# Kernel tuning notes

Hardware: AMD Instinct MI355X
Metric: run time of the kernel (lower is better)

Reference implementation:

```python
import jax, jax.numpy as jnp
import numpy as np

TOP_K = 2
NUM_EXPERTS = 64
AUX_COEF = 0.01


def setup_inputs() -> dict:
    key = jax.random.key(0)
    kx, kw = jax.random.split(key)
    B, S, D, E = 4, 4096, 2048, NUM_EXPERTS
    x = jax.random.normal(kx, (B, S, D), dtype=jnp.float32)
    # nn.Linear default init ~ U(-1/sqrt(D), 1/sqrt(D))
    W = jax.random.uniform(kw, (E, D), dtype=jnp.float32,
                           minval=-1.0 / np.sqrt(D), maxval=1.0 / np.sqrt(D))
    return {"x": x, "W": W}


def reference(x, W):
    B, S, D = x.shape
    E = W.shape[0]
    # router projection (no bias)
    logits = jnp.einsum('bsd,ed->bse', x, W)          # [B,S,E]
    probs = jax.nn.softmax(logits, axis=-1)           # [B,S,E]
    top_k_gates, top_k_indices = jax.lax.top_k(probs, TOP_K)  # [B,S,K]
    top_k_gates = top_k_gates / (jnp.sum(top_k_gates, axis=-1, keepdims=True) + 1e-9)
    # aux loss: fraction of routed slots per expert (one-hot mean) x mean router prob
    total_slots = B * S * TOP_K
    counts = jnp.zeros((E,), dtype=jnp.float32).at[top_k_indices.reshape(-1)].add(1.0)
    avg_tokens_per_expert = counts / total_slots      # == one_hot(idx).mean(dims 0,1,2)
    avg_router_prob = jnp.mean(probs, axis=(0, 1))    # [E]
    aux_loss = AUX_COEF * E * jnp.sum(avg_tokens_per_expert * avg_router_prob)
    return top_k_indices, top_k_gates, aux_loss
```

## Files before the change

### kernel.cpp

```cpp
#include <hip/hip_runtime.h>
#include <math.h>

#define NTOK 16384
#define DDIM 2048
#define NEXP 64
#define TM   16
#define NBLK (NTOK / TM)
#define NCH  32
#define NS   64

typedef _Float16 half4v __attribute__((ext_vector_type(4)));
typedef _Float16 half8v __attribute__((ext_vector_type(8)));
typedef float    f32x4  __attribute__((ext_vector_type(4)));

#define MFMA16(a, b, c) __builtin_amdgcn_mfma_f32_16x16x32_f16((a), (b), (c), 0, 0, 0)

__global__ __launch_bounds__(256) void prep_kernel(const float* __restrict__ W,
                                                   _Float16* __restrict__ Wh,
                                                   _Float16* __restrict__ Wl,
                                                   float* __restrict__ accg) {
    int idx = blockIdx.x * 256 + threadIdx.x;
    int e  = idx >> 8;
    int k0 = (idx & 255) << 3;
    const float* wp = W + (size_t)e * DDIM + k0;
    float4 w0 = *(const float4*)wp;
    float4 w1 = *(const float4*)(wp + 4);
    half8v h, l;
    h[0] = (_Float16)w0.x; l[0] = (_Float16)(w0.x - (float)h[0]);
    h[1] = (_Float16)w0.y; l[1] = (_Float16)(w0.y - (float)h[1]);
    h[2] = (_Float16)w0.z; l[2] = (_Float16)(w0.z - (float)h[2]);
    h[3] = (_Float16)w0.w; l[3] = (_Float16)(w0.w - (float)h[3]);
    h[4] = (_Float16)w1.x; l[4] = (_Float16)(w1.x - (float)h[4]);
    h[5] = (_Float16)w1.y; l[5] = (_Float16)(w1.y - (float)h[5]);
    h[6] = (_Float16)w1.z; l[6] = (_Float16)(w1.z - (float)h[6]);
    h[7] = (_Float16)w1.w; l[7] = (_Float16)(w1.w - (float)h[7]);
    int S = k0 >> 5, nb = e >> 4, nl = e & 15, q = (k0 >> 3) & 3;
    size_t off = (size_t)S * 2048 + nb * 512 + q * 128 + nl * 8;
    *(half8v*)&Wh[off] = h;
    *(half8v*)&Wl[off] = l;
    if (idx < 128) accg[idx] = 0.0f;
}

__device__ inline void cvt_store(_Float16* __restrict__ Hp, _Float16* __restrict__ Lp,
                                 int off, float4 v) {
    half4v h, l;
    h.x = (_Float16)v.x; l.x = (_Float16)(v.x - (float)h.x);
    h.y = (_Float16)v.y; l.y = (_Float16)(v.y - (float)h.y);
    h.z = (_Float16)v.z; l.z = (_Float16)(v.z - (float)h.z);
    h.w = (_Float16)v.w; l.w = (_Float16)(v.w - (float)h.w);
    *(half4v*)&Hp[off] = h;
    *(half4v*)&Lp[off] = l;
}

__global__ __launch_bounds__(256, 4) void router_kernel(
    const float* __restrict__ x, const _Float16* __restrict__ Wh,
    const _Float16* __restrict__ Wl, float* __restrict__ accg,
    float* __restrict__ out)
{
    __shared__ __align__(16) _Float16 Ah[2][1024];
    __shared__ __align__(16) _Float16 Al[2][1024];
    __shared__ float lgt[TM][NEXP + 1];
    __shared__ float cnt[NEXP];

    const int tid  = threadIdx.x;
    const int lane = tid & 63;
    const int wv   = __builtin_amdgcn_readfirstlane(tid >> 6);
    const int m0   = blockIdx.x * TM;

    if (tid < NEXP) cnt[tid] = 0.0f;

    const int tok0 = tid >> 4;
    const int kk0  = (tid & 15) * 4;
    const int s0   = kk0 >> 5, q0 = (kk0 >> 3) & 3, j00 = kk0 & 7;
    const int offA = (s0 * 64 + q0 * 16 + tok0) * 8 + j00;

    const float* gx = x + (size_t)(m0 + tok0) * DDIM + kk0;

    const _Float16* whp = Wh + wv * 512 + lane * 8;
    const _Float16* wlp = Wl + wv * 512 + lane * 8;

    f32x4 acc = {0.f, 0.f, 0.f, 0.f};

    float4 stg[4];
    #pragma unroll
    for (int i = 0; i < 4; ++i) stg[i] = *(const float4*)(gx + i * 64);
    half8v wbh[2], wbl[2];
    #pragma unroll
    for (int s = 0; s < 2; ++s) {
        wbh[s] = *(const half8v*)(whp + (size_t)s * 2048);
        wbl[s] = *(const half8v*)(wlp + (size_t)s * 2048);
    }

    for (int ch = 0; ch < NCH; ++ch) {
        const int p = ch & 1;
        const int b = ch & 3;
        cvt_store(&Ah[p][0], &Al[p][0], offA, stg[b]);
        const int cf = (ch + 4 < NCH) ? ch + 4 : 0;
        stg[b] = *(const float4*)(gx + cf * 64);
        asm volatile("s_waitcnt lgkmcnt(0)" ::: "memory");
        __builtin_amdgcn_s_barrier();
        #pragma unroll
        for (int s = 0; s < 2; ++s) {
            const int Sg  = ch * 2 + s;
            const int SgN = (Sg + 2) & (NS - 1);
            half8v ah = *(const half8v*)&Ah[p][(s * 64 + lane) * 8];
            half8v al = *(const half8v*)&Al[p][(s * 64 + lane) * 8];
            half8v bh = wbh[s], bl = wbl[s];
            wbh[s] = *(const half8v*)(whp + (size_t)SgN * 2048);
            wbl[s] = *(const half8v*)(wlp + (size_t)SgN * 2048);
            acc = MFMA16(al, bh, acc);
            acc = MFMA16(ah, bl, acc);
            acc = MFMA16(ah, bh, acc);
        }
    }

    {
        const int q  = lane >> 4;
        const int nl = lane & 15;
        #pragma unroll
        for (int r = 0; r < 4; ++r)
            lgt[q * 4 + r][wv * 16 + nl] = acc[r];
    }
    __syncthreads();

    if (tid < 128) {
        const int m = tid >> 3;
        const int j = tid & 7;
        float l[8];
        #pragma unroll
        for (int i = 0; i < 8; ++i) l[i] = lgt[m][j * 8 + i];

        float mx = l[0];
        #pragma unroll
        for (int i = 1; i < 8; ++i) mx = fmaxf(mx, l[i]);
        #pragma unroll
        for (int off = 1; off < 8; off <<= 1) mx = fmaxf(mx, __shfl_xor(mx, off, 8));

        float ev[8];
        float zs = 0.f;
        float v1 = -INFINITY, v2 = -INFINITY;
        int i1 = 0, i2 = 0;
        #pragma unroll
        for (int i = 0; i < 8; ++i) {
            ev[i] = __expf(l[i] - mx);
            zs += ev[i];
            int e = j * 8 + i;
            if (l[i] > v1)      { v2 = v1; i2 = i1; v1 = l[i]; i1 = e; }
            else if (l[i] > v2) { v2 = l[i]; i2 = e; }
        }
        #pragma unroll
        for (int off = 1; off < 8; off <<= 1) zs += __shfl_xor(zs, off, 8);

        #pragma unroll
        for (int off = 1; off < 8; off <<= 1) {
            float ov1 = __shfl_xor(v1, off, 8);
            int   oi1 = __shfl_xor(i1, off, 8);
            float ov2 = __shfl_xor(v2, off, 8);
            int   oi2 = __shfl_xor(i2, off, 8);
            bool afirst = (v1 > ov1) || (v1 == ov1 && i1 < oi1);
            if (afirst) {
                bool t = (v2 > ov1) || (v2 == ov1 && i2 < oi1);
                v2 = t ? v2 : ov1;
                i2 = t ? i2 : oi1;
            } else {
                bool t = (ov2 > v1) || (ov2 == v1 && oi2 < i1);
                v2 = t ? ov2 : v1;
                i2 = t ? oi2 : i1;
                v1 = ov1;
                i1 = oi1;
            }
        }

        const float invz = 1.0f / zs;
        if (j == 0) {
            float p1 = invz;
            float p2 = __expf(v2 - mx) * invz;
            float sden = p1 + p2 + 1e-9f;
            int tok = m0 + m;
            out[tok * 2 + 0] = (float)i1;
            out[tok * 2 + 1] = (float)i2;
            out[32768 + tok * 2 + 0] = p1 / sden;
            out[32768 + tok * 2 + 1] = p2 / sden;
            atomicAdd(&cnt[i1], 1.0f);
            atomicAdd(&cnt[i2], 1.0f);
        }

        #pragma unroll
        for (int i = 0; i < 8; ++i) lgt[m][j * 8 + i] = ev[i] * invz;
    }
    __syncthreads();

    if (tid < NEXP) {
        atomicAdd(&accg[tid], cnt[tid]);
    } else if (tid < 128) {
        int e = tid - 64;
        float s = 0.f;
        #pragma unroll
        for (int t = 0; t < TM; ++t) s += lgt[t][e];
        atomicAdd(&accg[64 + e], s);
    }
}

__global__ void finalize_kernel(const float* __restrict__ accg,
                                float* __restrict__ out)
{
    int t = threadIdx.x;
    float c = accg[t];
    float p = accg[64 + t];
    float term = (c / (float)(NTOK * 2)) * (p / (float)NTOK);
    #pragma unroll
    for (int off = 1; off < 64; off <<= 1) term += __shfl_xor(term, off, 64);
    if (t == 0) out[65536] = 0.01f * (float)NEXP * term;
}

extern "C" void kernel_launch(void* const* d_in, const int* in_sizes, int n_in,
                              void* d_out, int out_size, void* d_ws, size_t ws_size,
                              hipStream_t stream) {
    const float* x = (const float*)d_in[0];
    const float* W = (const float*)d_in[1];
    float* out  = (float*)d_out;
    float* accg = (float*)d_ws;
    _Float16* Wh = (_Float16*)(accg + 128);
    _Float16* Wl = Wh + (size_t)DDIM * NEXP;

    prep_kernel<<<64, 256, 0, stream>>>(W, Wh, Wl, accg);
    router_kernel<<<NBLK, 256, 0, stream>>>(x, Wh, Wl, accg, out);
    finalize_kernel<<<1, 64, 0, stream>>>(accg, out);
}
```

Baseline: 220.0 us.

## Load x directly into MFMA registers and split K across waves with LDS reduction

Each block now handles 32 tokens. Its four waves split into two token halves and two K halves, and each wave computes all 64 experts with four accumulators. The kernel drops the LDS staging of x and the per-chunk barriers: each lane loads its fp32 x fragment straight from global memory and converts it to hi/lo halves in registers. A final LDS pass adds the two K-half partial sums. The change removes barrier and LDS traffic and reuses each x fragment across four expert tiles, at the cost of more registers, lower occupancy (launch bounds drop to 2) and uncoalesced strided row loads of x.

```diff
diff --git a/kernel.cpp b/kernel.cpp
--- a/kernel.cpp
+++ b/kernel.cpp
@@ -4,12 +4,10 @@
 #define NTOK 16384
 #define DDIM 2048
 #define NEXP 64
-#define TM   16
-#define NBLK (NTOK / TM)
-#define NCH  32
-#define NS   64
-
-typedef _Float16 half4v __attribute__((ext_vector_type(4)));
+#define TMB  32
+#define NBLK (NTOK / TMB)
+#define NSW  32
+
 typedef _Float16 half8v __attribute__((ext_vector_type(8)));
 typedef float    f32x4  __attribute__((ext_vector_type(4)));
 
@@ -41,89 +39,117 @@
     if (idx < 128) accg[idx] = 0.0f;
 }
 
-__device__ inline void cvt_store(_Float16* __restrict__ Hp, _Float16* __restrict__ Lp,
-                                 int off, float4 v) {
-    half4v h, l;
-    h.x = (_Float16)v.x; l.x = (_Float16)(v.x - (float)h.x);
-    h.y = (_Float16)v.y; l.y = (_Float16)(v.y - (float)h.y);
-    h.z = (_Float16)v.z; l.z = (_Float16)(v.z - (float)h.z);
-    h.w = (_Float16)v.w; l.w = (_Float16)(v.w - (float)h.w);
-    *(half4v*)&Hp[off] = h;
-    *(half4v*)&Lp[off] = l;
-}
-
-__global__ __launch_bounds__(256, 4) void router_kernel(
+__global__ __launch_bounds__(256, 2) void router_kernel(
     const float* __restrict__ x, const _Float16* __restrict__ Wh,
     const _Float16* __restrict__ Wl, float* __restrict__ accg,
     float* __restrict__ out)
 {
-    __shared__ __align__(16) _Float16 Ah[2][1024];
-    __shared__ __align__(16) _Float16 Al[2][1024];
-    __shared__ float lgt[TM][NEXP + 1];
+    __shared__ float pacc[2][64][16];
+    __shared__ float lgt[TMB][NEXP + 1];
     __shared__ float cnt[NEXP];
 
     const int tid  = threadIdx.x;
     const int lane = tid & 63;
     const int wv   = __builtin_amdgcn_readfirstlane(tid >> 6);
-    const int m0   = blockIdx.x * TM;
+    const int th   = wv & 1;
+    const int qk   = wv >> 1;
+    const int m0   = blockIdx.x * TMB;
 
     if (tid < NEXP) cnt[tid] = 0.0f;
 
-    const int tok0 = tid >> 4;
-    const int kk0  = (tid & 15) * 4;
-    const int s0   = kk0 >> 5, q0 = (kk0 >> 3) & 3, j00 = kk0 & 7;
-    const int offA = (s0 * 64 + q0 * 16 + tok0) * 8 + j00;
-
-    const float* gx = x + (size_t)(m0 + tok0) * DDIM + kk0;
-
-    const _Float16* whp = Wh + wv * 512 + lane * 8;
-    const _Float16* wlp = Wl + wv * 512 + lane * 8;
-
-    f32x4 acc = {0.f, 0.f, 0.f, 0.f};
-
-    float4 stg[4];
-    #pragma unroll
-    for (int i = 0; i < 4; ++i) stg[i] = *(const float4*)(gx + i * 64);
-    half8v wbh[2], wbl[2];
-    #pragma unroll
-    for (int s = 0; s < 2; ++s) {
-        wbh[s] = *(const half8v*)(whp + (size_t)s * 2048);
-        wbl[s] = *(const half8v*)(wlp + (size_t)s * 2048);
-    }
-
-    for (int ch = 0; ch < NCH; ++ch) {
-        const int p = ch & 1;
-        const int b = ch & 3;
-        cvt_store(&Ah[p][0], &Al[p][0], offA, stg[b]);
-        const int cf = (ch + 4 < NCH) ? ch + 4 : 0;
-        stg[b] = *(const float4*)(gx + cf * 64);
-        asm volatile("s_waitcnt lgkmcnt(0)" ::: "memory");
-        __builtin_amdgcn_s_barrier();
-        #pragma unroll
-        for (int s = 0; s < 2; ++s) {
-            const int Sg  = ch * 2 + s;
-            const int SgN = (Sg + 2) & (NS - 1);
-            half8v ah = *(const half8v*)&Ah[p][(s * 64 + lane) * 8];
-            half8v al = *(const half8v*)&Al[p][(s * 64 + lane) * 8];
-            half8v bh = wbh[s], bl = wbl[s];
-            wbh[s] = *(const half8v*)(whp + (size_t)SgN * 2048);
-            wbl[s] = *(const half8v*)(wlp + (size_t)SgN * 2048);
-            acc = MFMA16(al, bh, acc);
-            acc = MFMA16(ah, bl, acc);
-            acc = MFMA16(ah, bh, acc);
-        }
-    }
+    const int row = m0 + th * 16 + (lane & 15);
+    const float* gxp = x + (size_t)row * DDIM + qk * 1024 + (lane >> 4) * 8;
+
+    const _Float16* wbh = Wh + (size_t)qk * (NSW * 2048) + lane * 8;
+    const _Float16* wbl = Wl + (size_t)qk * (NSW * 2048) + lane * 8;
+
+    f32x4 acc0 = {0.f,0.f,0.f,0.f}, acc1 = {0.f,0.f,0.f,0.f};
+    f32x4 acc2 = {0.f,0.f,0.f,0.f}, acc3 = {0.f,0.f,0.f,0.f};
+
+    float4 xA0 = *(const float4*)(gxp +   0), xB0 = *(const float4*)(gxp +   4);
+    float4 xA1 = *(const float4*)(gxp +  32), xB1 = *(const float4*)(gxp +  36);
+    float4 xA2 = *(const float4*)(gxp +  64), xB2 = *(const float4*)(gxp +  68);
+    float4 xA3 = *(const float4*)(gxp +  96), xB3 = *(const float4*)(gxp + 100);
+    half8v h0a = *(const half8v*)(wbh +    0), h1a = *(const half8v*)(wbh +  512);
+    half8v h2a = *(const half8v*)(wbh + 1024), h3a = *(const half8v*)(wbh + 1536);
+    half8v l0a = *(const half8v*)(wbl +    0), l1a = *(const half8v*)(wbl +  512);
+    half8v l2a = *(const half8v*)(wbl + 1024), l3a = *(const half8v*)(wbl + 1536);
+    half8v h0b = *(const half8v*)(wbh + 2048), h1b = *(const half8v*)(wbh + 2560);
+    half8v h2b = *(const half8v*)(wbh + 3072), h3b = *(const half8v*)(wbh + 3584);
+    half8v l0b = *(const half8v*)(wbl + 2048), l1b = *(const half8v*)(wbl + 2560);
+    half8v l2b = *(const half8v*)(wbl + 3072), l3b = *(const half8v*)(wbl + 3584);
+
+#define STEP(S, XA, XB, H0,H1,H2,H3, L0,L1,L2,L3)                           \
+    {                                                                        \
+        half8v ah, al;                                                       \
+        ah[0]=(_Float16)XA.x; al[0]=(_Float16)(XA.x-(float)ah[0]);           \
+        ah[1]=(_Float16)XA.y; al[1]=(_Float16)(XA.y-(float)ah[1]);           \
+        ah[2]=(_Float16)XA.z; al[2]=(_Float16)(XA.z-(float)ah[2]);           \
+        ah[3]=(_Float16)XA.w; al[3]=(_Float16)(XA.w-(float)ah[3]);           \
+        ah[4]=(_Float16)XB.x; al[4]=(_Float16)(XB.x-(float)ah[4]);           \
+        ah[5]=(_Float16)XB.y; al[5]=(_Float16)(XB.y-(float)ah[5]);           \
+        ah[6]=(_Float16)XB.z; al[6]=(_Float16)(XB.z-(float)ah[6]);           \
+        ah[7]=(_Float16)XB.w; al[7]=(_Float16)(XB.w-(float)ah[7]);           \
+        half8v bh0=H0, bl0=L0, bh1=H1, bl1=L1;                               \
+        half8v bh2=H2, bl2=L2, bh3=H3, bl3=L3;                               \
+        const int Sw_ = ((S) + 2 < NSW) ? (S) + 2 : 0;                       \
+        const _Float16* whs = wbh + (size_t)Sw_ * 2048;                      \
+        const _Float16* wls = wbl + (size_t)Sw_ * 2048;                      \
+        H0 = *(const half8v*)(whs +    0); L0 = *(const half8v*)(wls +    0);\
+        H1 = *(const half8v*)(whs +  512); L1 = *(const half8v*)(wls +  512);\
+        H2 = *(const half8v*)(whs + 1024); L2 = *(const half8v*)(wls + 1024);\
+        H3 = *(const half8v*)(whs + 1536); L3 = *(const half8v*)(wls + 1536);\
+        acc0 = MFMA16(al, bh0, acc0);                                        \
+        acc0 = MFMA16(ah, bl0, acc0);                                        \
+        acc0 = MFMA16(ah, bh0, acc0);                                        \
+        acc1 = MFMA16(al, bh1, acc1);                                        \
+        acc1 = MFMA16(ah, bl1, acc1);                                        \
+        acc1 = MFMA16(ah, bh1, acc1);                                        \
+        acc2 = MFMA16(al, bh2, acc2);                                        \
+        acc2 = MFMA16(ah, bl2, acc2);                                        \
+        acc2 = MFMA16(ah, bh2, acc2);                                        \
+        acc3 = MFMA16(al, bh3, acc3);                                        \
+        acc3 = MFMA16(ah, bl3, acc3);                                        \
+        acc3 = MFMA16(ah, bh3, acc3);                                        \
+        const int Sx_ = ((S) + 4 < NSW) ? (S) + 4 : 0;                       \
+        XA = *(const float4*)(gxp + Sx_ * 32);                               \
+        XB = *(const float4*)(gxp + Sx_ * 32 + 4);                           \
+    }
+
+    for (int s = 0; s < NSW; s += 4) {
+        STEP(s + 0, xA0, xB0, h0a,h1a,h2a,h3a, l0a,l1a,l2a,l3a);
+        STEP(s + 1, xA1, xB1, h0b,h1b,h2b,h3b, l0b,l1b,l2b,l3b);
+        STEP(s + 2, xA2, xB2, h0a,h1a,h2a,h3a, l0a,l1a,l2a,l3a);
+        STEP(s + 3, xA3, xB3, h0b,h1b,h2b,h3b, l0b,l1b,l2b,l3b);
+    }
+#undef STEP
+
+    if (wv >= 2) {
+        #pragma unroll
+        for (int r = 0; r < 4; ++r) {
+            pacc[th][lane][ 0 + r] = acc0[r];
+            pacc[th][lane][ 4 + r] = acc1[r];
+            pacc[th][lane][ 8 + r] = acc2[r];
+            pacc[th][lane][12 + r] = acc3[r];
+        }
+    }
+    __syncthreads();
+
+    if (wv < 2) {
+        const int qr = lane >> 4;
+        const int nl = lane & 15;
+        #pragma unroll
+        for (int r = 0; r < 4; ++r) {
+            const int m = th * 16 + qr * 4 + r;
+            lgt[m][ 0 + nl] = acc0[r] + pacc[th][lane][ 0 + r];
+            lgt[m][16 + nl] = acc1[r] + pacc[th][lane][ 4 + r];
+            lgt[m][32 + nl] = acc2[r] + pacc[th][lane][ 8 + r];
+            lgt[m][48 + nl] = acc3[r] + pacc[th][lane][12 + r];
+        }
+    }
+    __syncthreads();
 
     {
-        const int q  = lane >> 4;
-        const int nl = lane & 15;
-        #pragma unroll
-        for (int r = 0; r < 4; ++r)
-            lgt[q * 4 + r][wv * 16 + nl] = acc[r];
-    }
-    __syncthreads();
-
-    if (tid < 128) {
         const int m = tid >> 3;
         const int j = tid & 7;
         float l[8];
@@ -196,7 +222,7 @@
         int e = tid - 64;
         float s = 0.f;
         #pragma unroll
-        for (int t = 0; t < TM; ++t) s += lgt[t][e];
+        for (int t = 0; t < TMB; ++t) s += lgt[t][e];
         atomicAdd(&accg[64 + e], s);
     }
 }
```

Measured after the change: 227.5 us. 3.4% more time.

## Stage x and W tiles into LDS via direct global-to-LDS loads with 32-token blocks

Applied to the files above, without the earlier changes.

Raises tokens per block from 16 to 32 and gives each wave a 16x32 output tile, so every W fragment fetched into shared memory is reused across twice as many tokens. Both x (triple-buffered, fp32) and the hi/lo fp16 W (double-buffered) now move into LDS with global_load_lds, and the hi/lo split of x happens after the LDS read instead of before the store. This aims to cut W traffic per token and free registers from the staging loads. In exchange it uses much more LDS, lowers the occupancy hint to 2 blocks, and relies on hand-placed vmcnt waits.

```diff
diff --git a/kernel.cpp b/kernel.cpp
--- a/kernel.cpp
+++ b/kernel.cpp
@@ -4,16 +4,20 @@
 #define NTOK 16384
 #define DDIM 2048
 #define NEXP 64
-#define TM   16
-#define NBLK (NTOK / TM)
+#define TMB  32
+#define NBLK (NTOK / TMB)
 #define NCH  32
-#define NS   64
-
-typedef _Float16 half4v __attribute__((ext_vector_type(4)));
+
 typedef _Float16 half8v __attribute__((ext_vector_type(8)));
 typedef float    f32x4  __attribute__((ext_vector_type(4)));
 
 #define MFMA16(a, b, c) __builtin_amdgcn_mfma_f32_16x16x32_f16((a), (b), (c), 0, 0, 0)
+
+__device__ __forceinline__ void stage16(const void* g, void* l) {
+    __builtin_amdgcn_global_load_lds(
+        (const __attribute__((address_space(1))) unsigned int*)g,
+        (__attribute__((address_space(3))) unsigned int*)l, 16, 0, 0);
+}
 
 __global__ __launch_bounds__(256) void prep_kernel(const float* __restrict__ W,
                                                    _Float16* __restrict__ Wh,
@@ -41,89 +45,120 @@
     if (idx < 128) accg[idx] = 0.0f;
 }
 
-__device__ inline void cvt_store(_Float16* __restrict__ Hp, _Float16* __restrict__ Lp,
-                                 int off, float4 v) {
-    half4v h, l;
-    h.x = (_Float16)v.x; l.x = (_Float16)(v.x - (float)h.x);
-    h.y = (_Float16)v.y; l.y = (_Float16)(v.y - (float)h.y);
-    h.z = (_Float16)v.z; l.z = (_Float16)(v.z - (float)h.z);
-    h.w = (_Float16)v.w; l.w = (_Float16)(v.w - (float)h.w);
-    *(half4v*)&Hp[off] = h;
-    *(half4v*)&Lp[off] = l;
-}
-
-__global__ __launch_bounds__(256, 4) void router_kernel(
+__global__ __launch_bounds__(256, 2) void router_kernel(
     const float* __restrict__ x, const _Float16* __restrict__ Wh,
     const _Float16* __restrict__ Wl, float* __restrict__ accg,
     float* __restrict__ out)
 {
-    __shared__ __align__(16) _Float16 Ah[2][1024];
-    __shared__ __align__(16) _Float16 Al[2][1024];
-    __shared__ float lgt[TM][NEXP + 1];
+    __shared__ __align__(16) float    Xs[3][2048];
+    __shared__ __align__(16) _Float16 Ws[2][2][4096];
+    __shared__ float lgt[TMB][NEXP + 1];
     __shared__ float cnt[NEXP];
 
     const int tid  = threadIdx.x;
     const int lane = tid & 63;
     const int wv   = __builtin_amdgcn_readfirstlane(tid >> 6);
-    const int m0   = blockIdx.x * TM;
+    const int th   = wv & 1;
+    const int eh   = wv >> 1;
+    const int m0   = blockIdx.x * TMB;
 
     if (tid < NEXP) cnt[tid] = 0.0f;
 
-    const int tok0 = tid >> 4;
-    const int kk0  = (tid & 15) * 4;
-    const int s0   = kk0 >> 5, q0 = (kk0 >> 3) & 3, j00 = kk0 & 7;
-    const int offA = (s0 * 64 + q0 * 16 + tok0) * 8 + j00;
-
-    const float* gx = x + (size_t)(m0 + tok0) * DDIM + kk0;
-
-    const _Float16* whp = Wh + wv * 512 + lane * 8;
-    const _Float16* wlp = Wl + wv * 512 + lane * 8;
-
-    f32x4 acc = {0.f, 0.f, 0.f, 0.f};
-
-    float4 stg[4];
-    #pragma unroll
-    for (int i = 0; i < 4; ++i) stg[i] = *(const float4*)(gx + i * 64);
-    half8v wbh[2], wbl[2];
-    #pragma unroll
-    for (int s = 0; s < 2; ++s) {
-        wbh[s] = *(const half8v*)(whp + (size_t)s * 2048);
-        wbl[s] = *(const half8v*)(wlp + (size_t)s * 2048);
-    }
-
+    const int sth = wv >> 1, sst = wv & 1;
+    const float* gx0 = x + (size_t)(m0 + sth * 16 + (lane & 15)) * DDIM
+                         + sst * 32 + (lane >> 4) * 8;
+    const float* gx1 = gx0 + 4;
+    float* xdst0 = &Xs[0][(2 * wv) * 256];
+    float* xdst1 = &Xs[0][(2 * wv + 1) * 256];
+    const _Float16* wgsrc = (wv < 2 ? Wh : Wl) + (wv & 1) * 2048 + lane * 8;
+    _Float16* wdbase = &Ws[eh][0][(wv & 1) * 2048];
+
+#define STAGE_W(CW, BW)                                                      \
+    {                                                                        \
+        const _Float16* ws_ = wgsrc + (size_t)(CW) * 4096;                   \
+        _Float16* wd_ = wdbase + (BW) * 4096;                                \
+        stage16(ws_,        wd_);                                            \
+        stage16(ws_ +  512, wd_ +  512);                                     \
+        stage16(ws_ + 1024, wd_ + 1024);                                     \
+        stage16(ws_ + 1536, wd_ + 1536);                                     \
+    }
+#define STAGE_X(CS, BX)                                                      \
+    {                                                                        \
+        stage16(gx0 + (size_t)(CS) * 64, xdst0 + (BX) * 2048);               \
+        stage16(gx1 + (size_t)(CS) * 64, xdst1 + (BX) * 2048);               \
+    }
+
+    const float* xrd = &Xs[0][th * 1024 + lane * 4];
+    const _Float16* whrd = &Ws[0][0][eh * 1024 + lane * 8];
+    const _Float16* wlrd = &Ws[1][0][eh * 1024 + lane * 8];
+
+    f32x4 acc0 = {0.f, 0.f, 0.f, 0.f}, acc1 = {0.f, 0.f, 0.f, 0.f};
+
+    STAGE_W(0, 0);
+    STAGE_X(0, 0);
+    STAGE_X(1, 1);
+    __builtin_amdgcn_sched_barrier(0);
+    asm volatile("s_waitcnt vmcnt(2) lgkmcnt(0)" ::: "memory");
+    __builtin_amdgcn_s_barrier();
+    __builtin_amdgcn_sched_barrier(0);
+
+    int xb = 0, xsb = 2;
     for (int ch = 0; ch < NCH; ++ch) {
-        const int p = ch & 1;
-        const int b = ch & 3;
-        cvt_store(&Ah[p][0], &Al[p][0], offA, stg[b]);
-        const int cf = (ch + 4 < NCH) ? ch + 4 : 0;
-        stg[b] = *(const float4*)(gx + cf * 64);
-        asm volatile("s_waitcnt lgkmcnt(0)" ::: "memory");
+        const int wb = ch & 1;
+        int cw = ch + 1; if (cw >= NCH) cw = 0;
+        int cs = ch + 2; if (cs >= NCH) cs -= NCH;
+        STAGE_W(cw, wb ^ 1);
+        STAGE_X(cs, xsb);
+
+        #pragma unroll
+        for (int s = 0; s < 2; ++s) {
+            const float4 xa  = *(const float4*)(xrd + xb * 2048 + s * 512);
+            const float4 xbv = *(const float4*)(xrd + xb * 2048 + s * 512 + 256);
+            half8v ah, al;
+            ah[0]=(_Float16)xa.x;  al[0]=(_Float16)(xa.x -(float)ah[0]);
+            ah[1]=(_Float16)xa.y;  al[1]=(_Float16)(xa.y -(float)ah[1]);
+            ah[2]=(_Float16)xa.z;  al[2]=(_Float16)(xa.z -(float)ah[2]);
+            ah[3]=(_Float16)xa.w;  al[3]=(_Float16)(xa.w -(float)ah[3]);
+            ah[4]=(_Float16)xbv.x; al[4]=(_Float16)(xbv.x-(float)ah[4]);
+            ah[5]=(_Float16)xbv.y; al[5]=(_Float16)(xbv.y-(float)ah[5]);
+            ah[6]=(_Float16)xbv.z; al[6]=(_Float16)(xbv.z-(float)ah[6]);
+            ah[7]=(_Float16)xbv.w; al[7]=(_Float16)(xbv.w-(float)ah[7]);
+            half8v bh0 = *(const half8v*)(whrd + wb * 4096 + s * 2048);
+            half8v bl0 = *(const half8v*)(wlrd + wb * 4096 + s * 2048);
+            half8v bh1 = *(const half8v*)(whrd + wb * 4096 + s * 2048 + 512);
+            half8v bl1 = *(const half8v*)(wlrd + wb * 4096 + s * 2048 + 512);
+            acc0 = MFMA16(al, bh0, acc0);
+            acc0 = MFMA16(ah, bl0, acc0);
+            acc0 = MFMA16(ah, bh0, acc0);
+            acc1 = MFMA16(al, bh1, acc1);
+            acc1 = MFMA16(ah, bl1, acc1);
+            acc1 = MFMA16(ah, bh1, acc1);
+        }
+
+        __builtin_amdgcn_sched_barrier(0);
+        asm volatile("s_waitcnt vmcnt(2) lgkmcnt(0)" ::: "memory");
         __builtin_amdgcn_s_barrier();
-        #pragma unroll
-        for (int s = 0; s < 2; ++s) {
-            const int Sg  = ch * 2 + s;
-            const int SgN = (Sg + 2) & (NS - 1);
-            half8v ah = *(const half8v*)&Ah[p][(s * 64 + lane) * 8];
-            half8v al = *(const half8v*)&Al[p][(s * 64 + lane) * 8];
-            half8v bh = wbh[s], bl = wbl[s];
-            wbh[s] = *(const half8v*)(whp + (size_t)SgN * 2048);
-            wbl[s] = *(const half8v*)(wlp + (size_t)SgN * 2048);
-            acc = MFMA16(al, bh, acc);
-            acc = MFMA16(ah, bl, acc);
-            acc = MFMA16(ah, bh, acc);
-        }
-    }
+        __builtin_amdgcn_sched_barrier(0);
+
+        xb  = (xb  == 2) ? 0 : xb  + 1;
+        xsb = (xsb == 2) ? 0 : xsb + 1;
+    }
+#undef STAGE_W
+#undef STAGE_X
 
     {
-        const int q  = lane >> 4;
+        const int qr = lane >> 4;
         const int nl = lane & 15;
         #pragma unroll
-        for (int r = 0; r < 4; ++r)
-            lgt[q * 4 + r][wv * 16 + nl] = acc[r];
+        for (int r = 0; r < 4; ++r) {
+            const int m = th * 16 + qr * 4 + r;
+            lgt[m][(eh * 2 + 0) * 16 + nl] = acc0[r];
+            lgt[m][(eh * 2 + 1) * 16 + nl] = acc1[r];
+        }
     }
     __syncthreads();
 
-    if (tid < 128) {
+    {
         const int m = tid >> 3;
         const int j = tid & 7;
         float l[8];
@@ -196,7 +231,7 @@
         int e = tid - 64;
         float s = 0.f;
         #pragma unroll
-        for (int t = 0; t < TM; ++t) s += lgt[t][e];
+        for (int t = 0; t < TMB; ++t) s += lgt[t][e];
         atomicAdd(&accg[64 + e], s);
     }
 }
```

Result: slower. 226.1 us (+2.8%).

## Stage fp32 x tiles into swizzled LDS via direct global-to-LDS loads

Applied to the files above, without the earlier changes.

Replaces register-staged fp32 loads with in-loop fp16 hi/lo conversion and stores to LDS. x tiles now go straight to LDS with global_load_lds, in 256-wide K chunks that are double-buffered and XOR-swizzled. Each wave reads fp32 from LDS and does the hi/lo split just before the MFMAs. Per chunk this cuts register pressure and issues fewer, larger barriers. In exchange, all four waves redundantly convert the same A fragments, and the weight fragments lose their register prefetch, so W loads are issued right before use.

```diff
diff --git a/kernel.cpp b/kernel.cpp
--- a/kernel.cpp
+++ b/kernel.cpp
@@ -6,14 +6,20 @@
 #define NEXP 64
 #define TM   16
 #define NBLK (NTOK / TM)
-#define NCH  32
-#define NS   64
-
-typedef _Float16 half4v __attribute__((ext_vector_type(4)));
+#define KCH  256
+#define NCH  (DDIM / KCH)
+#define SPC  (KCH / 32)
+
 typedef _Float16 half8v __attribute__((ext_vector_type(8)));
 typedef float    f32x4  __attribute__((ext_vector_type(4)));
 
 #define MFMA16(a, b, c) __builtin_amdgcn_mfma_f32_16x16x32_f16((a), (b), (c), 0, 0, 0)
+
+__device__ __forceinline__ void stage16(const void* g, void* l) {
+    __builtin_amdgcn_global_load_lds(
+        (const __attribute__((address_space(1))) unsigned int*)g,
+        (__attribute__((address_space(3))) unsigned int*)l, 16, 0, 0);
+}
 
 __global__ __launch_bounds__(256) void prep_kernel(const float* __restrict__ W,
                                                    _Float16* __restrict__ Wh,
@@ -41,24 +47,12 @@
     if (idx < 128) accg[idx] = 0.0f;
 }
 
-__device__ inline void cvt_store(_Float16* __restrict__ Hp, _Float16* __restrict__ Lp,
-                                 int off, float4 v) {
-    half4v h, l;
-    h.x = (_Float16)v.x; l.x = (_Float16)(v.x - (float)h.x);
-    h.y = (_Float16)v.y; l.y = (_Float16)(v.y - (float)h.y);
-    h.z = (_Float16)v.z; l.z = (_Float16)(v.z - (float)h.z);
-    h.w = (_Float16)v.w; l.w = (_Float16)(v.w - (float)h.w);
-    *(half4v*)&Hp[off] = h;
-    *(half4v*)&Lp[off] = l;
-}
-
 __global__ __launch_bounds__(256, 4) void router_kernel(
     const float* __restrict__ x, const _Float16* __restrict__ Wh,
     const _Float16* __restrict__ Wl, float* __restrict__ accg,
     float* __restrict__ out)
 {
-    __shared__ __align__(16) _Float16 Ah[2][1024];
-    __shared__ __align__(16) _Float16 Al[2][1024];
+    __shared__ __align__(16) float Xs[2][4096];
     __shared__ float lgt[TM][NEXP + 1];
     __shared__ float cnt[NEXP];
 
@@ -69,49 +63,56 @@
 
     if (tid < NEXP) cnt[tid] = 0.0f;
 
-    const int tok0 = tid >> 4;
-    const int kk0  = (tid & 15) * 4;
-    const int s0   = kk0 >> 5, q0 = (kk0 >> 3) & 3, j00 = kk0 & 7;
-    const int offA = (s0 * 64 + q0 * 16 + tok0) * 8 + j00;
-
-    const float* gx = x + (size_t)(m0 + tok0) * DDIM + kk0;
+    const float* xrow0 = x + (size_t)(m0 +  0 + wv) * DDIM + ((((lane * 16) ^ (((     wv) & 7) << 4))) >> 2);
+    const float* xrow1 = x + (size_t)(m0 +  4 + wv) * DDIM + ((((lane * 16) ^ ((( 4 + wv) & 7) << 4))) >> 2);
+    const float* xrow2 = x + (size_t)(m0 +  8 + wv) * DDIM + ((((lane * 16) ^ ((( 8 + wv) & 7) << 4))) >> 2);
+    const float* xrow3 = x + (size_t)(m0 + 12 + wv) * DDIM + ((((lane * 16) ^ (((12 + wv) & 7) << 4))) >> 2);
 
     const _Float16* whp = Wh + wv * 512 + lane * 8;
     const _Float16* wlp = Wl + wv * 512 + lane * 8;
 
+    const int row = lane & 15;
+    const int swz = (row & 7) << 4;
+    const int kb0 = (lane >> 4) * 32;
+
     f32x4 acc = {0.f, 0.f, 0.f, 0.f};
 
-    float4 stg[4];
-    #pragma unroll
-    for (int i = 0; i < 4; ++i) stg[i] = *(const float4*)(gx + i * 64);
-    half8v wbh[2], wbl[2];
-    #pragma unroll
-    for (int s = 0; s < 2; ++s) {
-        wbh[s] = *(const half8v*)(whp + (size_t)s * 2048);
-        wbl[s] = *(const half8v*)(wlp + (size_t)s * 2048);
-    }
-
-    for (int ch = 0; ch < NCH; ++ch) {
-        const int p = ch & 1;
-        const int b = ch & 3;
-        cvt_store(&Ah[p][0], &Al[p][0], offA, stg[b]);
-        const int cf = (ch + 4 < NCH) ? ch + 4 : 0;
-        stg[b] = *(const float4*)(gx + cf * 64);
-        asm volatile("s_waitcnt lgkmcnt(0)" ::: "memory");
-        __builtin_amdgcn_s_barrier();
-        #pragma unroll
-        for (int s = 0; s < 2; ++s) {
-            const int Sg  = ch * 2 + s;
-            const int SgN = (Sg + 2) & (NS - 1);
-            half8v ah = *(const half8v*)&Ah[p][(s * 64 + lane) * 8];
-            half8v al = *(const half8v*)&Al[p][(s * 64 + lane) * 8];
-            half8v bh = wbh[s], bl = wbl[s];
-            wbh[s] = *(const half8v*)(whp + (size_t)SgN * 2048);
-            wbl[s] = *(const half8v*)(wlp + (size_t)SgN * 2048);
+    stage16(xrow0, &Xs[0][0 * 1024 + wv * 256]);
+    stage16(xrow1, &Xs[0][1 * 1024 + wv * 256]);
+    stage16(xrow2, &Xs[0][2 * 1024 + wv * 256]);
+    stage16(xrow3, &Xs[0][3 * 1024 + wv * 256]);
+    __syncthreads();
+
+    for (int c = 0; c < NCH; ++c) {
+        const int b  = c & 1;
+        const int cn = (c + 1) & (NCH - 1);
+        stage16(xrow0 + cn * KCH, &Xs[b ^ 1][0 * 1024 + wv * 256]);
+        stage16(xrow1 + cn * KCH, &Xs[b ^ 1][1 * 1024 + wv * 256]);
+        stage16(xrow2 + cn * KCH, &Xs[b ^ 1][2 * 1024 + wv * 256]);
+        stage16(xrow3 + cn * KCH, &Xs[b ^ 1][3 * 1024 + wv * 256]);
+
+        const char* xb = (const char*)&Xs[b][0];
+        #pragma unroll
+        for (int s = 0; s < SPC; ++s) {
+            const int Sg = c * SPC + s;
+            const float4 xa = *(const float4*)(xb + row * 1024 + ((s * 128 + kb0) ^ swz));
+            const float4 xc = *(const float4*)(xb + row * 1024 + ((s * 128 + kb0 + 16) ^ swz));
+            half8v ah, al;
+            ah[0]=(_Float16)xa.x; al[0]=(_Float16)(xa.x-(float)ah[0]);
+            ah[1]=(_Float16)xa.y; al[1]=(_Float16)(xa.y-(float)ah[1]);
+            ah[2]=(_Float16)xa.z; al[2]=(_Float16)(xa.z-(float)ah[2]);
+            ah[3]=(_Float16)xa.w; al[3]=(_Float16)(xa.w-(float)ah[3]);
+            ah[4]=(_Float16)xc.x; al[4]=(_Float16)(xc.x-(float)ah[4]);
+            ah[5]=(_Float16)xc.y; al[5]=(_Float16)(xc.y-(float)ah[5]);
+            ah[6]=(_Float16)xc.z; al[6]=(_Float16)(xc.z-(float)ah[6]);
+            ah[7]=(_Float16)xc.w; al[7]=(_Float16)(xc.w-(float)ah[7]);
+            const half8v bh = *(const half8v*)(whp + (size_t)Sg * 2048);
+            const half8v bl = *(const half8v*)(wlp + (size_t)Sg * 2048);
             acc = MFMA16(al, bh, acc);
             acc = MFMA16(ah, bl, acc);
             acc = MFMA16(ah, bh, acc);
         }
+        __syncthreads();
     }
 
     {
```

After: 233.2 us. 1.06x slower.
